# Optimization experiments

Hardware: AMD Instinct MI355X
Metric: run time of the kernel (lower is better)

Reference implementation:

```python
import jax, jax.numpy as jnp
import numpy as np

N_NODES = 50000
N_EDGES = 800000
NODE_DIM = 3
EDGE_DIM = 32
HIDDEN = 128
NUM_GRAPHS = 256


def _linear_init(key, fan_in, fan_out):
    # torch nn.Linear default: U(-1/sqrt(fan_in), 1/sqrt(fan_in))
    kw, kb = jax.random.split(key)
    bound = 1.0 / np.sqrt(fan_in)
    W = jax.random.uniform(kw, (fan_in, fan_out), jnp.float32, -bound, bound)
    b = jax.random.uniform(kb, (fan_out,), jnp.float32, -bound, bound)
    return W, b


def setup_inputs() -> dict:
    key = jax.random.key(0)
    ks = jax.random.split(key, 16)
    x = jax.random.normal(ks[0], (N_NODES, NODE_DIM), jnp.float32)
    edge_index = jax.random.randint(ks[1], (2, N_EDGES), 0, N_NODES, jnp.int64)
    edge_attr = jax.random.uniform(ks[2], (N_EDGES, EDGE_DIM), jnp.float32)
    batch = jnp.sort(jax.random.randint(ks[3], (N_NODES,), 0, NUM_GRAPHS, jnp.int64))

    # conv1: CGConv(channels=3, dim=32) -> lin_f, lin_s: (2*3+32) -> 3
    Wf1, bf1 = _linear_init(ks[4], 2 * NODE_DIM + EDGE_DIM, NODE_DIM)
    Ws1, bs1 = _linear_init(ks[5], 2 * NODE_DIM + EDGE_DIM, NODE_DIM)
    # node_proj: 3 -> 128
    Wp, bp = _linear_init(ks[6], NODE_DIM, HIDDEN)
    zin = 2 * HIDDEN + EDGE_DIM
    Wf_list, bf_list, Ws_list, bs_list = [], [], [], []
    for i in range(2):
        Wf, bf = _linear_init(ks[7 + i], zin, HIDDEN)
        Ws, bs = _linear_init(ks[9 + i], zin, HIDDEN)
        Wf_list.append(Wf); bf_list.append(bf); Ws_list.append(Ws); bs_list.append(bs)
    Wf_convs = jnp.stack(Wf_list); bf_convs = jnp.stack(bf_list)
    Ws_convs = jnp.stack(Ws_list); bs_convs = jnp.stack(bs_list)
    # fc1: 128 -> 128
    W1, b1 = _linear_init(ks[11], HIDDEN, HIDDEN)
    # 5 heads: 128 -> 1, stacked as (5, 128) and (5,)
    Wh_list, bh_list = [], []
    for i in range(5):
        Wh, bh = _linear_init(jax.random.fold_in(ks[12], i), HIDDEN, 1)
        Wh_list.append(Wh[:, 0]); bh_list.append(bh[0])
    W_heads = jnp.stack(Wh_list)  # (5, 128)
    b_heads = jnp.stack(bh_list)  # (5,)

    return dict(x=x, edge_index=edge_index, edge_attr=edge_attr, batch=batch,
                Wf1=Wf1, bf1=bf1, Ws1=Ws1, bs1=bs1, Wp=Wp, bp=bp,
                Wf_convs=Wf_convs, bf_convs=bf_convs, Ws_convs=Ws_convs, bs_convs=bs_convs,
                W1=W1, b1=b1, W_heads=W_heads, b_heads=b_heads)


def _cgconv(x, src, dst, edge_attr, Wf, bf, Ws, bs):
    # PyG CGConv: z_ij = [x_i || x_j || e_ij], messages aggregated to i (dst)
    z = jnp.concatenate([x[dst], x[src], edge_attr], axis=-1)  # [E, 2C+D]
    msg = jax.nn.sigmoid(z @ Wf + bf) * jax.nn.softplus(z @ Ws + bs)  # [E, C]
    agg = jax.ops.segment_sum(msg, dst, num_segments=x.shape[0])
    return x + agg


def reference(x, edge_index, edge_attr, batch,
              Wf1, bf1, Ws1, bs1, Wp, bp,
              Wf_convs, bf_convs, Ws_convs, bs_convs,
              W1, b1, W_heads, b_heads):
    src, dst = edge_index[0], edge_index[1]
    h = _cgconv(x, src, dst, edge_attr, Wf1, bf1, Ws1, bs1)
    h = jax.nn.relu(h @ Wp + bp)
    for l in range(Wf_convs.shape[0]):
        h = _cgconv(h, src, dst, edge_attr, Wf_convs[l], bf_convs[l], Ws_convs[l], bs_convs[l])
        h = jax.nn.relu(h)
    # global mean pool over graphs
    sums = jax.ops.segment_sum(h, batch, num_segments=NUM_GRAPHS)
    counts = jax.ops.segment_sum(jnp.ones((h.shape[0],), h.dtype), batch, num_segments=NUM_GRAPHS)
    g = sums / jnp.maximum(counts, 1.0)[:, None]  # [G, H]
    g = jax.nn.relu(g @ W1 + b1)
    # 5 heads stacked -> [G, 5] (columns: volume, band_gap, formation_energy, density, bulk_modulus)
    out = g @ W_heads.T + b_heads
    return out
```

## Files before the change

kernel.cpp:

```cpp
#include <hip/hip_runtime.h>
#include <hip/hip_bf16.h>
#include <math.h>

#define N_NODES 50000
#define N_EDGES 800000
#define NODE_DIM 3
#define EDGE_DIM 32
#define HIDDEN 128
#define NUM_GRAPHS 256
#define ZIN (2*HIDDEN + EDGE_DIM)
#define NPAD 50176

typedef __attribute__((ext_vector_type(8))) short short8;
typedef __attribute__((ext_vector_type(4))) float f32x4;

__device__ __forceinline__ unsigned short f2bf(float x) {
    unsigned u = __float_as_uint(x);
    u += 0x7FFFu + ((u >> 16) & 1u);
    return (unsigned short)(u >> 16);
}
__device__ __forceinline__ float bf_lo(unsigned u) { return __uint_as_float(u << 16); }
__device__ __forceinline__ float bf_hi(unsigned u) { return __uint_as_float(u & 0xFFFF0000u); }

__global__ __launch_bounds__(256) void conv1_sorted_kernel(
    const float* __restrict__ x, const float* __restrict__ EA,
    const int4* __restrict__ epack,
    const float* __restrict__ Wf1, const float* __restrict__ bf1,
    const float* __restrict__ Ws1, const float* __restrict__ bs1,
    float* __restrict__ agg0)
{
    __shared__ float WfL[38*3], WsL[38*3], bfL[3], bsL[3];
    __shared__ float msgL[256*4];
    __shared__ int   pdL[256];

    if (threadIdx.x < 114) {
        WfL[threadIdx.x] = Wf1[threadIdx.x];
        WsL[threadIdx.x] = Ws1[threadIdx.x];
    }
    if (threadIdx.x < 3) { bfL[threadIdx.x] = bf1[threadIdx.x]; bsL[threadIdx.x] = bs1[threadIdx.x]; }
    __syncthreads();

    const int p = blockIdx.x * 256 + threadIdx.x;
    int4 e = epack[p];
    const int eid = e.x, s = e.y, d = e.z;
    pdL[threadIdx.x] = d;

    float z[38];
    z[0] = x[d*3+0]; z[1] = x[d*3+1]; z[2] = x[d*3+2];
    z[3] = x[s*3+0]; z[4] = x[s*3+1]; z[5] = x[s*3+2];
    const float4* ep = (const float4*)(EA + (size_t)eid * EDGE_DIM);
    #pragma unroll
    for (int q = 0; q < 8; ++q) {
        float4 v = ep[q];
        z[6+4*q+0] = v.x; z[6+4*q+1] = v.y; z[6+4*q+2] = v.z; z[6+4*q+3] = v.w;
    }
    float f[3], g[3];
    #pragma unroll
    for (int c = 0; c < 3; ++c) { f[c] = bfL[c]; g[c] = bsL[c]; }
    #pragma unroll
    for (int j = 0; j < 38; ++j) {
        #pragma unroll
        for (int c = 0; c < 3; ++c) {
            f[c] += z[j] * WfL[j*3+c];
            g[c] += z[j] * WsL[j*3+c];
        }
    }
    #pragma unroll
    for (int c = 0; c < 3; ++c) {
        float sig = __builtin_amdgcn_rcpf(1.0f + __expf(-f[c]));
        float sp  = fmaxf(g[c], 0.0f) + __logf(1.0f + __expf(-fabsf(g[c])));
        msgL[threadIdx.x*4 + c] = sig * sp;
    }
    __syncthreads();

    if (threadIdx.x < 48) {
        const int c   = threadIdx.x % 3;
        const int seg = threadIdx.x / 3;
        const int base = seg * 16;
        float acc = 0.0f;
        int cur = pdL[base];
        #pragma unroll 4
        for (int i = 0; i < 16; ++i) {
            int dd = pdL[base + i];
            float v = msgL[(base + i)*4 + c];
            if (dd != cur) {
                atomicAdd(agg0 + (size_t)cur*3 + c, acc);
                acc = 0.0f; cur = dd;
            }
            acc += v;
        }
        atomicAdd(agg0 + (size_t)cur*3 + c, acc);
    }
}

__global__ __launch_bounds__(256) void proj_kernel(
    const float* __restrict__ x, const float* __restrict__ agg0,
    const float* __restrict__ Wp, const float* __restrict__ bp,
    float* __restrict__ H)
{
    int idx = blockIdx.x * 256 + threadIdx.x;
    if (idx >= N_NODES * HIDDEN) return;
    int n = idx >> 7, c = idx & 127;
    float h0 = x[n*3+0] + agg0[n*3+0];
    float h1 = x[n*3+1] + agg0[n*3+1];
    float h2 = x[n*3+2] + agg0[n*3+2];
    float v = bp[c] + h0*Wp[0*128+c] + h1*Wp[1*128+c] + h2*Wp[2*128+c];
    H[idx] = fmaxf(v, 0.0f);
}

__global__ __launch_bounds__(256) void hist_kernel(
    const int* __restrict__ ei, int* __restrict__ hist)
{
    int e = blockIdx.x * 256 + threadIdx.x;
    if (e < N_EDGES) atomicAdd(&hist[ei[N_EDGES + e]], 1);
}

__global__ __launch_bounds__(256) void scanA_kernel(
    const int* __restrict__ hist, int* __restrict__ cursor, int* __restrict__ btot)
{
    __shared__ int tmp[256];
    int t = threadIdx.x;
    int i = blockIdx.x * 256 + t;
    int v = hist[i];
    tmp[t] = v;
    __syncthreads();
    #pragma unroll
    for (int off = 1; off < 256; off <<= 1) {
        int y = (t >= off) ? tmp[t - off] : 0;
        __syncthreads();
        if (t >= off) tmp[t] += y;
        __syncthreads();
    }
    cursor[i] = tmp[t] - v;
    if (t == 255) btot[blockIdx.x] = tmp[t];
}

__global__ __launch_bounds__(256) void scanB_kernel(int* __restrict__ btot)
{
    __shared__ int tmp[256];
    int t = threadIdx.x;
    int v = btot[t];
    tmp[t] = v;
    __syncthreads();
    #pragma unroll
    for (int off = 1; off < 256; off <<= 1) {
        int y = (t >= off) ? tmp[t - off] : 0;
        __syncthreads();
        if (t >= off) tmp[t] += y;
        __syncthreads();
    }
    btot[t] = tmp[t] - v;
}

__global__ __launch_bounds__(256) void scanC_kernel(
    int* __restrict__ cursor, const int* __restrict__ btot)
{
    int i = blockIdx.x * 256 + threadIdx.x;
    cursor[i] += btot[blockIdx.x];
}

__global__ __launch_bounds__(256) void scatter_kernel(
    const int* __restrict__ ei, int* __restrict__ cursor,
    int4* __restrict__ epack)
{
    int e = blockIdx.x * 256 + threadIdx.x;
    if (e >= N_EDGES) return;
    int s = ei[e];
    int d = ei[N_EDGES + e];
    int p = atomicAdd(&cursor[d], 1);
    epack[p] = make_int4(e, s, d, 0);
}

__global__ __launch_bounds__(256) void repack_frag_kernel(
    const float* __restrict__ Wf, const float* __restrict__ Ws,
    unsigned short* __restrict__ Bfrag)
{
    int idx = blockIdx.x * 256 + threadIdx.x;
    if (idx >= 2*32*4*64) return;
    int lane = idx & 63;
    int kc   = (idx >> 6) & 3;
    int nt   = (idx >> 8) & 31;
    int l    = idx >> 13;
    const float* wf  = Wf + (size_t)l * ZIN * HIDDEN;
    const float* wsp = Ws + (size_t)l * ZIN * HIDDEN;
    int n = nt*16 + (lane & 15);
    int half = n >> 8;
    int within = n & 255;
    int cc = within >> 1;
    int t = within & 1;
    const float* W = t ? wsp : wf;
    unsigned short vals[8];
    #pragma unroll
    for (int j = 0; j < 8; ++j) {
        int k = kc*32 + (lane >> 4)*8 + j;
        vals[j] = f2bf(W[(size_t)(half*128 + k)*128 + cc]);
    }
    *(short8*)(Bfrag + (size_t)idx * 8) = *(short8*)vals;
}

__global__ __launch_bounds__(256) void repack_edge_frag_kernel(
    const float* __restrict__ Wf, const float* __restrict__ Ws,
    unsigned short* __restrict__ BE)
{
    int idx = blockIdx.x * 256 + threadIdx.x;
    if (idx >= 2*16*64) return;
    int lane = idx & 63;
    int nt   = (idx >> 6) & 15;
    int l    = idx >> 10;
    const float* W = ((nt & 8) ? Ws : Wf) + (size_t)l * ZIN * HIDDEN + 256*128;
    int c = (nt & 7)*16 + (lane & 15);
    unsigned short vals[8];
    #pragma unroll
    for (int j = 0; j < 8; ++j) {
        int k = (lane >> 4)*8 + j;
        vals[j] = f2bf(W[(size_t)k*128 + c]);
    }
    *(short8*)(BE + (size_t)idx * 8) = *(short8*)vals;
}

__global__ __launch_bounds__(256) void gemm_mfma(
    const float* __restrict__ H, const float* __restrict__ aggIn,
    const unsigned short* __restrict__ Bfrag,
    const float* __restrict__ bf, const float* __restrict__ bs,
    unsigned short* __restrict__ Pb)
{
    const int lane = threadIdx.x & 63;
    const int wave = threadIdx.x >> 6;
    const int m    = lane & 15;
    const int quad = lane >> 4;
    const int rowA = blockIdx.y * 64 + wave * 16 + m;
    const int colBase = blockIdx.x * 256;

    const float* hrow = H + (size_t)rowA * 128;
    short8 a[4];
    #pragma unroll
    for (int kc = 0; kc < 4; ++kc) {
        float4 v0 = *(const float4*)(hrow + kc*32 + quad*8);
        float4 v1 = *(const float4*)(hrow + kc*32 + quad*8 + 4);
        if (aggIn) {
            const float* arow = aggIn + (size_t)rowA * 128;
            float4 a0 = *(const float4*)(arow + kc*32 + quad*8);
            float4 a1 = *(const float4*)(arow + kc*32 + quad*8 + 4);
            v0.x = fmaxf(v0.x + a0.x, 0.f); v0.y = fmaxf(v0.y + a0.y, 0.f);
            v0.z = fmaxf(v0.z + a0.z, 0.f); v0.w = fmaxf(v0.w + a0.w, 0.f);
            v1.x = fmaxf(v1.x + a1.x, 0.f); v1.y = fmaxf(v1.y + a1.y, 0.f);
            v1.z = fmaxf(v1.z + a1.z, 0.f); v1.w = fmaxf(v1.w + a1.w, 0.f);
        }
        unsigned short t[8];
        t[0]=f2bf(v0.x); t[1]=f2bf(v0.y); t[2]=f2bf(v0.z); t[3]=f2bf(v0.w);
        t[4]=f2bf(v1.x); t[5]=f2bf(v1.y); t[6]=f2bf(v1.z); t[7]=f2bf(v1.w);
        a[kc] = *(short8*)t;
    }

    f32x4 acc[16];
    #pragma unroll
    for (int nt = 0; nt < 16; ++nt) {
        float bias = 0.0f;
        if (colBase == 0) {
            int col = nt*16 + m;
            bias = (col & 1) ? bs[col >> 1] : bf[col >> 1];
        }
        acc[nt] = (f32x4){bias, bias, bias, bias};
    }

    #pragma unroll
    for (int nt = 0; nt < 16; ++nt) {
        int ntg = (colBase >> 4) + nt;
        const unsigned short* bp = Bfrag + ((size_t)(ntg*4) * 64 + lane) * 8;
        #pragma unroll
        for (int kc = 0; kc < 4; ++kc) {
            short8 b = *(const short8*)(bp + (size_t)kc * 64 * 8);
            acc[nt] = __builtin_amdgcn_mfma_f32_16x16x32_bf16(a[kc], b, acc[nt], 0, 0, 0);
        }
    }

    const int rowC = blockIdx.y * 64 + wave * 16 + quad * 4;
    #pragma unroll
    for (int nt = 0; nt < 16; ++nt) {
        int col = colBase + nt*16 + m;
        #pragma unroll
        for (int r = 0; r < 4; ++r) {
            int row = rowC + r;
            if (row < N_NODES) Pb[(size_t)row * 512 + col] = f2bf(acc[nt][r]);
        }
    }
}

__global__ __launch_bounds__(256) void edge_kernel(
    const unsigned short* __restrict__ Pb, const float* __restrict__ EA,
    const int4* __restrict__ epack,
    const unsigned short* __restrict__ BE,
    float* __restrict__ agg)
{
    __shared__ float msgL[64*132];
    __shared__ int pdL[64];

    if (threadIdx.x < 64) pdL[threadIdx.x] = epack[blockIdx.x*64 + threadIdx.x].z;

    const int lane = threadIdx.x & 63;
    const int wave = threadIdx.x >> 6;
    const int m    = lane & 15;
    const int quad = lane >> 4;
    const int p0   = blockIdx.x * 64 + wave * 16;

    int eid = epack[p0 + m].x;
    const float* ea = EA + (size_t)eid * EDGE_DIM + quad*8;
    float4 v0 = *(const float4*)ea;
    float4 v1 = *(const float4*)(ea + 4);
    unsigned short t[8];
    t[0]=f2bf(v0.x); t[1]=f2bf(v0.y); t[2]=f2bf(v0.z); t[3]=f2bf(v0.w);
    t[4]=f2bf(v1.x); t[5]=f2bf(v1.y); t[6]=f2bf(v1.z); t[7]=f2bf(v1.w);
    short8 a = *(short8*)t;

    int dr[4], sr[4];
    #pragma unroll
    for (int r = 0; r < 4; ++r) {
        int4 e = epack[p0 + quad*4 + r];
        sr[r] = e.y; dr[r] = e.z;
    }

    const short8* BEv = (const short8*)BE;
    const f32x4 zero = (f32x4){0.f, 0.f, 0.f, 0.f};
    #pragma unroll
    for (int nt = 0; nt < 8; ++nt) {
        short8 bF = BEv[nt*64 + lane];
        short8 bS = BEv[(nt+8)*64 + lane];
        f32x4 qf = __builtin_amdgcn_mfma_f32_16x16x32_bf16(a, bF, zero, 0, 0, 0);
        f32x4 qs = __builtin_amdgcn_mfma_f32_16x16x32_bf16(a, bS, zero, 0, 0, 0);
        int c = nt*16 + m;
        #pragma unroll
        for (int r = 0; r < 4; ++r) {
            unsigned pd = *(const unsigned*)(Pb + (size_t)dr[r]*512 + 2*c);
            unsigned ps = *(const unsigned*)(Pb + (size_t)sr[r]*512 + 256 + 2*c);
            float f = bf_lo(pd) + bf_lo(ps) + qf[r];
            float g = bf_hi(pd) + bf_hi(ps) + qs[r];
            float sig = __builtin_amdgcn_rcpf(1.0f + __expf(-f));
            float sp  = fmaxf(g, 0.0f) + __logf(1.0f + __expf(-fabsf(g)));
            msgL[(wave*16 + quad*4 + r)*132 + c] = sig * sp;
        }
    }
    __syncthreads();

    const int c2  = threadIdx.x & 127;
    const int seg = threadIdx.x >> 7;
    const int base = seg * 32;
    float acc = 0.0f;
    int cur = pdL[base];
    #pragma unroll 4
    for (int i = 0; i < 32; ++i) {
        int dd = pdL[base + i];
        float v = msgL[(base + i)*132 + c2];
        if (dd != cur) {
            atomicAdd(&agg[(size_t)cur * HIDDEN + c2], acc);
            acc = 0.0f; cur = dd;
        }
        acc += v;
    }
    atomicAdd(&agg[(size_t)cur * HIDDEN + c2], acc);
}

__global__ __launch_bounds__(128) void pool_kernel(
    const float* __restrict__ H, const float* __restrict__ agg1,
    const float* __restrict__ agg2, const int* __restrict__ batch,
    float* __restrict__ gsum, float* __restrict__ gcnt)
{
    const int c = threadIdx.x;
    const int n0 = blockIdx.x * 128;
    float acc = 0.0f;
    int cur = -1;
    for (int i = 0; i < 128; ++i) {
        int n = n0 + i;
        if (n >= N_NODES) break;
        int g = batch[n];
        if (g != cur) {
            if (cur >= 0) atomicAdd(gsum + (size_t)cur * HIDDEN + c, acc);
            cur = g; acc = 0.0f;
        }
        size_t ix = (size_t)n * HIDDEN + c;
        float h = fmaxf(fmaxf(H[ix] + agg1[ix], 0.0f) + agg2[ix], 0.0f);
        acc += h;
    }
    if (cur >= 0) atomicAdd(gsum + (size_t)cur * HIDDEN + c, acc);

    if (c == 0) {
        int curg = -1; float run = 0.0f;
        for (int i = 0; i < 128; ++i) {
            int n = n0 + i;
            if (n >= N_NODES) break;
            int g = batch[n];
            if (g != curg) {
                if (curg >= 0) atomicAdd(gcnt + curg, run);
                curg = g; run = 0.0f;
            }
            run += 1.0f;
        }
        if (curg >= 0) atomicAdd(gcnt + curg, run);
    }
}

__global__ __launch_bounds__(128) void head_kernel(
    const float* __restrict__ gsum, const float* __restrict__ gcnt,
    const float* __restrict__ W1, const float* __restrict__ b1,
    const float* __restrict__ Wh, const float* __restrict__ bh,
    float* __restrict__ out)
{
    __shared__ float gavg[128];
    __shared__ float g1[128];
    const int g = blockIdx.x, c = threadIdx.x;
    float cnt = fmaxf(gcnt[g], 1.0f);
    gavg[c] = gsum[(size_t)g * HIDDEN + c] / cnt;
    __syncthreads();
    float acc = b1[c];
    for (int k = 0; k < 128; ++k) acc += gavg[k] * W1[k*128 + c];
    g1[c] = fmaxf(acc, 0.0f);
    __syncthreads();
    if (c < 5) {
        float o = bh[c];
        for (int k = 0; k < 128; ++k) o += g1[k] * Wh[c*128 + k];
        out[(size_t)g * 5 + c] = o;
    }
}

extern "C" void kernel_launch(void* const* d_in, const int* in_sizes, int n_in,
                              void* d_out, int out_size, void* d_ws, size_t ws_size,
                              hipStream_t stream) {
    const float* x        = (const float*)d_in[0];
    const int*   ei       = (const int*)  d_in[1];
    const float* EA       = (const float*)d_in[2];
    const int*   batch    = (const int*)  d_in[3];
    const float* Wf1      = (const float*)d_in[4];
    const float* bf1      = (const float*)d_in[5];
    const float* Ws1      = (const float*)d_in[6];
    const float* bs1      = (const float*)d_in[7];
    const float* Wp       = (const float*)d_in[8];
    const float* bp       = (const float*)d_in[9];
    const float* Wf_convs = (const float*)d_in[10];
    const float* bf_convs = (const float*)d_in[11];
    const float* Ws_convs = (const float*)d_in[12];
    const float* bs_convs = (const float*)d_in[13];
    const float* W1       = (const float*)d_in[14];
    const float* b1       = (const float*)d_in[15];
    const float* W_heads  = (const float*)d_in[16];
    const float* b_heads  = (const float*)d_in[17];
    float* out = (float*)d_out;

    float* ws = (float*)d_ws;
    float* agg0 = ws + 0;
    float* H    = ws + 150016;
    unsigned short* Pb = (unsigned short*)(ws + 6550016);
    float* agg1 = ws + 19350016;
    float* agg2 = ws + 25750016;
    unsigned short* Bfrag = (unsigned short*)(ws + 32150016);
    unsigned short* BE    = (unsigned short*)(ws + 32215552);
    float* gsum = ws + 32223744;
    float* gcnt = ws + 32256512;
    int* hist   = (int*)(ws + 32257024);
    int* cursor = (int*)(ws + 32307200);
    int* btot   = (int*)(ws + 32357376);
    int4* epack = (int4*)(ws + 32357632);

    hipMemsetAsync(hist, 0, (size_t)(2*NPAD + 256) * sizeof(int), stream);
    hist_kernel<<<(N_EDGES + 255)/256, 256, 0, stream>>>(ei, hist);
    scanA_kernel<<<NPAD/256, 256, 0, stream>>>(hist, cursor, btot);
    scanB_kernel<<<1, 256, 0, stream>>>(btot);
    scanC_kernel<<<NPAD/256, 256, 0, stream>>>(cursor, btot);
    scatter_kernel<<<(N_EDGES + 255)/256, 256, 0, stream>>>(ei, cursor, epack);

    hipMemsetAsync(agg0, 0, (size_t)N_NODES * 3 * sizeof(float), stream);
    conv1_sorted_kernel<<<N_EDGES/256, 256, 0, stream>>>(x, EA, epack, Wf1, bf1, Ws1, bs1, agg0);
    proj_kernel<<<(N_NODES*HIDDEN + 255)/256, 256, 0, stream>>>(x, agg0, Wp, bp, H);
    repack_frag_kernel<<<(2*32*4*64 + 255)/256, 256, 0, stream>>>(Wf_convs, Ws_convs, Bfrag);
    repack_edge_frag_kernel<<<(2*16*64 + 255)/256, 256, 0, stream>>>(Wf_convs, Ws_convs, BE);

    dim3 ggrid(2, (N_NODES + 63)/64);
    gemm_mfma<<<ggrid, 256, 0, stream>>>(H, nullptr, Bfrag, bf_convs, bs_convs, Pb);
    hipMemsetAsync(agg1, 0, (size_t)N_NODES * HIDDEN * sizeof(float), stream);
    edge_kernel<<<N_EDGES/64, 256, 0, stream>>>(Pb, EA, epack, BE, agg1);
    gemm_mfma<<<ggrid, 256, 0, stream>>>(H, agg1, Bfrag + (size_t)32*4*64*8,
                                         bf_convs + HIDDEN, bs_convs + HIDDEN, Pb);
    hipMemsetAsync(agg2, 0, (size_t)N_NODES * HIDDEN * sizeof(float), stream);
    edge_kernel<<<N_EDGES/64, 256, 0, stream>>>(Pb, EA, epack, BE + (size_t)16*64*8, agg2);

    hipMemsetAsync(gsum, 0, (size_t)(NUM_GRAPHS * HIDDEN + NUM_GRAPHS) * sizeof(float), stream);
    pool_kernel<<<(N_NODES + 127)/128, 128, 0, stream>>>(H, agg1, agg2, batch, gsum, gcnt);
    head_kernel<<<NUM_GRAPHS, 128, 0, stream>>>(gsum, gcnt, W1, b1, W_heads, b_heads, out);
}
```

Baseline: 699.1 us.

## Fold log2e into weights and use native exp2/log2 in gated messages

Pre-scales the filter and softplus weights and biases by log2(e) so the sigmoid and softplus can call the hardware exp2/log2 intrinsics directly, without the extra multiplies that __expf/__logf add. The messages therefore come out scaled by log2(e), and every consumer of the aggregates (proj, the GEMM A-load, pooling) corrects this with an fma by ln2. The edge kernel also precomputes gather and LDS row pointers, and replaces the per-iteration destination compare in the segmented reduction with a ballot-built boundary bitmask. The bitmask reads the neighbouring pdL entry straight after writing it, with no barrier in between, which relies on in-order LDS access within one wave.

```diff
diff --git a/kernel.cpp b/kernel.cpp
--- a/kernel.cpp
+++ b/kernel.cpp
@@ -11,6 +11,9 @@
 #define ZIN (2*HIDDEN + EDGE_DIM)
 #define NPAD 50176
 
+#define LOG2E 1.44269504088896f
+#define LN2   0.69314718055995f
+
 typedef __attribute__((ext_vector_type(8))) short short8;
 typedef __attribute__((ext_vector_type(4))) float f32x4;
 
@@ -34,10 +37,13 @@
     __shared__ int   pdL[256];
 
     if (threadIdx.x < 114) {
-        WfL[threadIdx.x] = Wf1[threadIdx.x];
-        WsL[threadIdx.x] = Ws1[threadIdx.x];
-    }
-    if (threadIdx.x < 3) { bfL[threadIdx.x] = bf1[threadIdx.x]; bsL[threadIdx.x] = bs1[threadIdx.x]; }
+        WfL[threadIdx.x] = Wf1[threadIdx.x] * LOG2E;
+        WsL[threadIdx.x] = Ws1[threadIdx.x] * LOG2E;
+    }
+    if (threadIdx.x < 3) {
+        bfL[threadIdx.x] = bf1[threadIdx.x] * LOG2E;
+        bsL[threadIdx.x] = bs1[threadIdx.x] * LOG2E;
+    }
     __syncthreads();
 
     const int p = blockIdx.x * 256 + threadIdx.x;
@@ -67,8 +73,8 @@
     }
     #pragma unroll
     for (int c = 0; c < 3; ++c) {
-        float sig = __builtin_amdgcn_rcpf(1.0f + __expf(-f[c]));
-        float sp  = fmaxf(g[c], 0.0f) + __logf(1.0f + __expf(-fabsf(g[c])));
+        float sig = __builtin_amdgcn_rcpf(1.0f + __builtin_amdgcn_exp2f(-f[c]));
+        float sp  = fmaxf(g[c], 0.0f) + __builtin_amdgcn_logf(1.0f + __builtin_amdgcn_exp2f(-fabsf(g[c])));
         msgL[threadIdx.x*4 + c] = sig * sp;
     }
     __syncthreads();
@@ -101,9 +107,9 @@
     int idx = blockIdx.x * 256 + threadIdx.x;
     if (idx >= N_NODES * HIDDEN) return;
     int n = idx >> 7, c = idx & 127;
-    float h0 = x[n*3+0] + agg0[n*3+0];
-    float h1 = x[n*3+1] + agg0[n*3+1];
-    float h2 = x[n*3+2] + agg0[n*3+2];
+    float h0 = fmaf(agg0[n*3+0], LN2, x[n*3+0]);
+    float h1 = fmaf(agg0[n*3+1], LN2, x[n*3+1]);
+    float h2 = fmaf(agg0[n*3+2], LN2, x[n*3+2]);
     float v = bp[c] + h0*Wp[0*128+c] + h1*Wp[1*128+c] + h2*Wp[2*128+c];
     H[idx] = fmaxf(v, 0.0f);
 }
@@ -193,7 +199,7 @@
     #pragma unroll
     for (int j = 0; j < 8; ++j) {
         int k = kc*32 + (lane >> 4)*8 + j;
-        vals[j] = f2bf(W[(size_t)(half*128 + k)*128 + cc]);
+        vals[j] = f2bf(W[(size_t)(half*128 + k)*128 + cc] * LOG2E);
     }
     *(short8*)(Bfrag + (size_t)idx * 8) = *(short8*)vals;
 }
@@ -213,7 +219,7 @@
     #pragma unroll
     for (int j = 0; j < 8; ++j) {
         int k = (lane >> 4)*8 + j;
-        vals[j] = f2bf(W[(size_t)k*128 + c]);
+        vals[j] = f2bf(W[(size_t)k*128 + c] * LOG2E);
     }
     *(short8*)(BE + (size_t)idx * 8) = *(short8*)vals;
 }
@@ -241,10 +247,10 @@
             const float* arow = aggIn + (size_t)rowA * 128;
             float4 a0 = *(const float4*)(arow + kc*32 + quad*8);
             float4 a1 = *(const float4*)(arow + kc*32 + quad*8 + 4);
-            v0.x = fmaxf(v0.x + a0.x, 0.f); v0.y = fmaxf(v0.y + a0.y, 0.f);
-            v0.z = fmaxf(v0.z + a0.z, 0.f); v0.w = fmaxf(v0.w + a0.w, 0.f);
-            v1.x = fmaxf(v1.x + a1.x, 0.f); v1.y = fmaxf(v1.y + a1.y, 0.f);
-            v1.z = fmaxf(v1.z + a1.z, 0.f); v1.w = fmaxf(v1.w + a1.w, 0.f);
+        v0.x = fmaxf(fmaf(a0.x, LN2, v0.x), 0.f); v0.y = fmaxf(fmaf(a0.y, LN2, v0.y), 0.f);
+        v0.z = fmaxf(fmaf(a0.z, LN2, v0.z), 0.f); v0.w = fmaxf(fmaf(a0.w, LN2, v0.w), 0.f);
+        v1.x = fmaxf(fmaf(a1.x, LN2, v1.x), 0.f); v1.y = fmaxf(fmaf(a1.y, LN2, v1.y), 0.f);
+        v1.z = fmaxf(fmaf(a1.z, LN2, v1.z), 0.f); v1.w = fmaxf(fmaf(a1.w, LN2, v1.w), 0.f);
         }
         unsigned short t[8];
         t[0]=f2bf(v0.x); t[1]=f2bf(v0.y); t[2]=f2bf(v0.z); t[3]=f2bf(v0.w);
@@ -258,7 +264,7 @@
         float bias = 0.0f;
         if (colBase == 0) {
             int col = nt*16 + m;
-            bias = (col & 1) ? bs[col >> 1] : bf[col >> 1];
+            bias = ((col & 1) ? bs[col >> 1] : bf[col >> 1]) * LOG2E;
         }
         acc[nt] = (f32x4){bias, bias, bias, bias};
     }
@@ -294,8 +300,16 @@
 {
     __shared__ float msgL[64*132];
     __shared__ int pdL[64];
-
-    if (threadIdx.x < 64) pdL[threadIdx.x] = epack[blockIdx.x*64 + threadIdx.x].z;
+    __shared__ unsigned bmask[2];
+
+    if (threadIdx.x < 64) {
+        const int t = threadIdx.x;
+        int d = epack[blockIdx.x*64 + t].z;
+        pdL[t] = d;
+        bool b = (t & 31) ? (d != pdL[t-1]) : false;
+        unsigned long long bal = __ballot(b);
+        if (t == 0) { bmask[0] = (unsigned)bal; bmask[1] = (unsigned)(bal >> 32); }
+    }
 
     const int lane = threadIdx.x & 63;
     const int wave = threadIdx.x >> 6;
@@ -312,11 +326,15 @@
     t[4]=f2bf(v1.x); t[5]=f2bf(v1.y); t[6]=f2bf(v1.z); t[7]=f2bf(v1.w);
     short8 a = *(short8*)t;
 
-    int dr[4], sr[4];
+    const unsigned short* pdp[4];
+    const unsigned short* psp[4];
+    float* mrow[4];
     #pragma unroll
     for (int r = 0; r < 4; ++r) {
         int4 e = epack[p0 + quad*4 + r];
-        sr[r] = e.y; dr[r] = e.z;
+        pdp[r] = Pb + (size_t)e.z * 512 + 2*m;
+        psp[r] = Pb + (size_t)e.y * 512 + 256 + 2*m;
+        mrow[r] = &msgL[(wave*16 + quad*4 + r)*132 + m];
     }
 
     const short8* BEv = (const short8*)BE;
@@ -327,16 +345,15 @@
         short8 bS = BEv[(nt+8)*64 + lane];
         f32x4 qf = __builtin_amdgcn_mfma_f32_16x16x32_bf16(a, bF, zero, 0, 0, 0);
         f32x4 qs = __builtin_amdgcn_mfma_f32_16x16x32_bf16(a, bS, zero, 0, 0, 0);
-        int c = nt*16 + m;
         #pragma unroll
         for (int r = 0; r < 4; ++r) {
-            unsigned pd = *(const unsigned*)(Pb + (size_t)dr[r]*512 + 2*c);
-            unsigned ps = *(const unsigned*)(Pb + (size_t)sr[r]*512 + 256 + 2*c);
+            unsigned pd = *(const unsigned*)(pdp[r] + nt*32);
+            unsigned ps = *(const unsigned*)(psp[r] + nt*32);
             float f = bf_lo(pd) + bf_lo(ps) + qf[r];
             float g = bf_hi(pd) + bf_hi(ps) + qs[r];
-            float sig = __builtin_amdgcn_rcpf(1.0f + __expf(-f));
-            float sp  = fmaxf(g, 0.0f) + __logf(1.0f + __expf(-fabsf(g)));
-            msgL[(wave*16 + quad*4 + r)*132 + c] = sig * sp;
+            float sig = __builtin_amdgcn_rcpf(1.0f + __builtin_amdgcn_exp2f(-f));
+            float sp  = fmaxf(g, 0.0f) + __builtin_amdgcn_logf(1.0f + __builtin_amdgcn_exp2f(-fabsf(g)));
+            mrow[r][nt*16] = sig * sp;
         }
     }
     __syncthreads();
@@ -344,19 +361,20 @@
     const int c2  = threadIdx.x & 127;
     const int seg = threadIdx.x >> 7;
     const int base = seg * 32;
+    unsigned msk = bmask[seg];
+    const float* mcol = &msgL[base*132 + c2];
     float acc = 0.0f;
-    int cur = pdL[base];
     #pragma unroll 4
     for (int i = 0; i < 32; ++i) {
-        int dd = pdL[base + i];
-        float v = msgL[(base + i)*132 + c2];
-        if (dd != cur) {
-            atomicAdd(&agg[(size_t)cur * HIDDEN + c2], acc);
-            acc = 0.0f; cur = dd;
-        }
+        float v = mcol[i*132];
+        if (msk & 1u) {
+            atomicAdd(&agg[(size_t)pdL[base + i - 1] * HIDDEN + c2], acc);
+            acc = 0.0f;
+        }
+        msk >>= 1;
         acc += v;
     }
-    atomicAdd(&agg[(size_t)cur * HIDDEN + c2], acc);
+    atomicAdd(&agg[(size_t)pdL[base + 31] * HIDDEN + c2], acc);
 }
 
 __global__ __launch_bounds__(128) void pool_kernel(
@@ -377,7 +395,7 @@
             cur = g; acc = 0.0f;
         }
         size_t ix = (size_t)n * HIDDEN + c;
-        float h = fmaxf(fmaxf(H[ix] + agg1[ix], 0.0f) + agg2[ix], 0.0f);
+        float h = fmaxf(fmaf(agg2[ix], LN2, fmaxf(fmaf(agg1[ix], LN2, H[ix]), 0.0f)), 0.0f);
         acc += h;
     }
     if (cur >= 0) atomicAdd(gsum + (size_t)cur * HIDDEN + c, acc);
```

Result: faster. 662.1 us (-5.3%).
